# Kernel optimization log

Hardware: AMD Instinct MI355X
Metric: run time of the kernel (lower is better)

Reference implementation:

```python
import jax, jax.numpy as jnp
import numpy as np

B, G, N, C = 4, 64, 256, 256
HEAD = 8
HD = C // HEAD  # 32


def setup_inputs() -> dict:
    key = jax.random.key(0)
    ks = jax.random.split(key, 11)
    s = 0.02
    return {
        "q": jax.random.normal(ks[0], (B, G, N, C), jnp.float32),
        "k": jax.random.normal(ks[1], (B, G, N, C), jnp.float32),
        "v": jax.random.normal(ks[2], (B, G, N, C), jnp.float32),
        "wq": jax.random.normal(ks[3], (C, C), jnp.float32) * s,
        "bq": jnp.zeros((C,), jnp.float32),
        "wk": jax.random.normal(ks[4], (C, C), jnp.float32) * s,
        "bk": jnp.zeros((C,), jnp.float32),
        "wv": jax.random.normal(ks[5], (C, C), jnp.float32) * s,
        "bv": jnp.zeros((C,), jnp.float32),
        "wo": jax.random.normal(ks[6], (C, C), jnp.float32) * s,
        "bo": jnp.zeros((C,), jnp.float32),
    }


def reference(q, k, v, wq, bq, wk, bk, wv, bv, wo, bo):
    # Linear projections (torch Linear == x @ W.T + b; here W stored as (in,out))
    Q = q @ wq + bq  # (B,G,N,C)
    K = k @ wk + bk
    V = v @ wv + bv
    # split heads: (B,G,N,C) -> (B,G,N,H,hd)
    Qh = Q.reshape(B, G, N, HEAD, HD)
    Kh = K.reshape(B, G, N, HEAD, HD)
    Vh = V.reshape(B, G, N, HEAD, HD)
    scale = jnp.sqrt(jnp.float32(HD)) + 1e-8
    # scores: per batch b, head h, group g: (N,N)
    score = jnp.einsum("bgnhd,bgmhd->bhgnm", Qh, Kh) / scale
    attn = jax.nn.softmax(score, axis=-1)
    ctx = jnp.einsum("bhgnm,bgmhd->bgnhd", attn, Vh)  # (B,G,N,H,hd)
    ctx = ctx.reshape(B, G, N, C)
    # output projection (dropout = identity in eval)
    return ctx @ wo + bo
```

## Files before the change

### kernel.cpp

```cpp
#include <hip/hip_runtime.h>
#include <hip/hip_bf16.h>
#include <cstdint>
#include <cstddef>


typedef __attribute__((ext_vector_type(4))) float f4;
typedef __attribute__((ext_vector_type(8))) short s8;
typedef __attribute__((ext_vector_type(4))) short s4;
typedef unsigned short u16;

#define AS1 __attribute__((address_space(1)))
#define AS3 __attribute__((address_space(3)))

static constexpr int CD = 256;

__device__ __forceinline__ u16 f2bf(float f) {
    __hip_bfloat16 h = __float2bfloat16(f);
    return *reinterpret_cast<u16*>(&h);
}

__device__ __forceinline__ void gload_lds16(const void* g, void* l) {
    __builtin_amdgcn_global_load_lds((const AS1 uint32_t*)g, (AS3 uint32_t*)l, 16, 0, 0);
}

__global__ __launch_bounds__(256) void prep_k(const float* __restrict__ wq,
                                              const float* __restrict__ wk,
                                              const float* __restrict__ wv,
                                              const float* __restrict__ wo,
                                              u16* __restrict__ WT, float qs)
{
    const int bx = blockIdx.x;
    const int wsel = bx >> 4, tl = bx & 15;
    const int k0 = (tl & 3) * 64, n0 = (tl >> 2) * 64;
    const float* W = wsel == 0 ? wq : wsel == 1 ? wk : wsel == 2 ? wv : wo;
    const float scale = wsel == 0 ? qs : 1.0f;
    u16* dst = WT + (size_t)wsel * 65536;
    __shared__ float T[64][65];
    const int t = threadIdx.x;
    const int rr = t >> 4, c0 = (t & 15) * 4;
    #pragma unroll
    for (int i = 0; i < 4; ++i) {
        int r = i * 16 + rr;
        f4 f = *(const f4*)(W + (size_t)(k0 + r) * CD + n0 + c0);
        #pragma unroll
        for (int j = 0; j < 4; ++j) T[c0 + j][r] = f[j] * scale;
    }
    __syncthreads();
    #pragma unroll
    for (int i = 0; i < 4; ++i) {
        int n = i * 16 + rr;
        s4 h;
        #pragma unroll
        for (int j = 0; j < 4; ++j) h[j] = (short)f2bf(T[n][c0 + j]);
        *(s4*)(dst + (size_t)(n0 + n) * CD + k0 + c0) = h;
    }
}

template<bool A_F32, bool OUT_F32>
__device__ __forceinline__ void gemm_body(const void* __restrict__ Ain,
                                          const u16* __restrict__ Wt,
                                          const float* __restrict__ bias,
                                          float escale, void* __restrict__ Out,
                                          int d)
{
    __shared__ u16 As[128 * 64];
    __shared__ u16 Bs[128 * 64];
    const int n0 = (d >> 9) * 128;
    const int m0 = (d & 511) * 128;
    const int t = threadIdx.x, lane = t & 63, w = t >> 6;
    const int wr = (w >> 1) * 64, wc = (w & 1) * 64;
    const int lr = lane & 15, lk = (lane >> 4) * 8;

    f4 acc[4][4] = {};

    for (int k0 = 0; k0 < CD; k0 += 64) {
        #pragma unroll
        for (int j = 0; j < 4; ++j) {
            int c = j * 4 + w;
            int row = c * 8 + (lane >> 3);
            int col = ((lane & 7) * 8) ^ ((row & 7) << 3);
            gload_lds16(Wt + (size_t)(n0 + row) * CD + k0 + col,
                        &Bs[c * 512 + lane * 8]);
        }
        if constexpr (A_F32) {
            const float* A = (const float*)Ain;
            #pragma unroll
            for (int j = 0; j < 4; ++j) {
                int ch = t + j * 256;
                int r = ch >> 3, c8 = ch & 7;
                const float* src = A + (size_t)(m0 + r) * CD + k0 + c8 * 8;
                f4 f0 = *(const f4*)src;
                f4 f1 = *(const f4*)(src + 4);
                s8 h;
                #pragma unroll
                for (int i = 0; i < 4; ++i) {
                    h[i]     = (short)f2bf(f0[i]);
                    h[i + 4] = (short)f2bf(f1[i]);
                }
                *(s8*)&As[r * 64 + ((c8 * 8) ^ ((r & 7) << 3))] = h;
            }
        } else {
            const u16* A = (const u16*)Ain;
            #pragma unroll
            for (int j = 0; j < 4; ++j) {
                int c = j * 4 + w;
                int row = c * 8 + (lane >> 3);
                int col = ((lane & 7) * 8) ^ ((row & 7) << 3);
                gload_lds16(A + (size_t)(m0 + row) * CD + k0 + col,
                            &As[c * 512 + lane * 8]);
            }
        }
        __syncthreads();

        #pragma unroll
        for (int kk = 0; kk < 64; kk += 32) {
            s8 a[4], b[4];
            #pragma unroll
            for (int m = 0; m < 4; ++m) {
                int R = wr + m * 16 + lr;
                a[m] = *(const s8*)&As[R * 64 + ((kk + lk) ^ ((R & 7) << 3))];
            }
            #pragma unroll
            for (int n = 0; n < 4; ++n) {
                int R = wc + n * 16 + lr;
                b[n] = *(const s8*)&Bs[R * 64 + ((kk + lk) ^ ((R & 7) << 3))];
            }
            #pragma unroll
            for (int m = 0; m < 4; ++m)
                #pragma unroll
                for (int n = 0; n < 4; ++n)
                    acc[m][n] = __builtin_amdgcn_mfma_f32_16x16x32_bf16(
                        a[m], b[n], acc[m][n], 0, 0, 0);
        }
        __syncthreads();
    }

    const int orow = (lane >> 4) * 4;
    #pragma unroll
    for (int n = 0; n < 4; ++n) {
        int col = n0 + wc + n * 16 + lr;
        float bb = bias[col] * escale;
        #pragma unroll
        for (int m = 0; m < 4; ++m)
            #pragma unroll
            for (int r = 0; r < 4; ++r) {
                int row = m0 + wr + m * 16 + orow + r;
                float v = acc[m][n][r] + bb;
                if constexpr (OUT_F32)
                    ((float*)Out)[(size_t)row * CD + col] = v;
                else
                    ((u16*)Out)[(size_t)row * CD + col] = f2bf(v);
            }
    }
}

__global__ __launch_bounds__(256, 3) void gemmqkv_k(const float* q, const float* k,
        const float* v, const u16* WT, const float* bq, const float* bk,
        const float* bv, float qs, u16* Qb, u16* Kb, u16* Vb)
{
    const int op = blockIdx.x >> 10;
    const int d  = blockIdx.x & 1023;
    const float* A    = op == 0 ? q  : op == 1 ? k  : v;
    const u16*   Wt   = WT + (size_t)op * 65536;
    const float* bias = op == 0 ? bq : op == 1 ? bk : bv;
    u16*         Out  = op == 0 ? Qb : op == 1 ? Kb : Vb;
    gemm_body<true, false>(A, Wt, bias, op == 0 ? qs : 1.0f, Out, d);
}

__global__ __launch_bounds__(256, 3) void gemmo_k(const u16* Cx, const u16* WT,
                                                  const float* bo, float* out)
{
    gemm_body<false, true>(Cx, WT, bo, 1.0f, out, blockIdx.x);
}

__global__ __launch_bounds__(256, 3) void attn_k(const u16* Qb,
                                                 const u16* __restrict__ Kb,
                                                 const u16* __restrict__ Vb,
                                                 u16* Ctx)
{
    __shared__ u16 Ks[256 * 32];
    __shared__ u16 Vt[32][260];
    __shared__ u16 Ps[4][16][132];
    const int d = blockIdx.x;
    const int bg = d & 255, h = d >> 8;
    const size_t base = (size_t)bg * (256 * 256) + h * 32;
    const int t = threadIdx.x, lane = t & 63, w = t >> 6;
    const int lr = lane & 15, lk = (lane >> 4) * 8;
    const int orow = (lane >> 4) * 4;

    #pragma unroll
    for (int j = 0; j < 4; ++j) {
        int c = j * 4 + w;
        int row = c * 16 + (lane >> 2);
        int col = ((lane & 3) * 8) ^ (((row >> 1) & 3) << 3);
        gload_lds16(Kb + base + (size_t)row * CD + col, &Ks[c * 512 + lane * 8]);
    }
    {
        int n0 = (t >> 2) * 4, c0 = (t & 3) * 8;
        const u16* vp = Vb + base + (size_t)n0 * CD + c0;
        s8 r0 = *(const s8*)(vp);
        s8 r1 = *(const s8*)(vp + CD);
        s8 r2 = *(const s8*)(vp + 2 * CD);
        s8 r3 = *(const s8*)(vp + 3 * CD);
        #pragma unroll
        for (int i = 0; i < 8; ++i) {
            s4 cv = { r0[i], r1[i], r2[i], r3[i] };
            *(s4*)&Vt[c0 + i][n0] = cv;
        }
    }
    s8 aq[4];
    #pragma unroll
    for (int m = 0; m < 4; ++m)
        aq[m] = *(const s8*)(Qb + base + (size_t)(w * 64 + m * 16 + lr) * CD + lk);

    __syncthreads();

    const int myslot = lk ^ (((lr >> 1) & 3) << 3);
    const f4 zero = {0.f, 0.f, 0.f, 0.f};

    #pragma unroll
    for (int m = 0; m < 4; ++m) {
        f4 s[16];
        #pragma unroll
        for (int j = 0; j < 16; ++j) {
            s8 bk = *(const s8*)&Ks[(j * 16 + lr) * 32 + myslot];
            s[j] = __builtin_amdgcn_mfma_f32_16x16x32_bf16(aq[m], bk, zero, 0, 0, 0);
        }
        float mrow[4] = {-3.0e38f, -3.0e38f, -3.0e38f, -3.0e38f};
        #pragma unroll
        for (int j = 0; j < 16; ++j)
            #pragma unroll
            for (int r = 0; r < 4; ++r) mrow[r] = fmaxf(mrow[r], s[j][r]);
        #pragma unroll
        for (int dd = 1; dd < 16; dd <<= 1)
            #pragma unroll
            for (int r = 0; r < 4; ++r) mrow[r] = fmaxf(mrow[r], __shfl_xor(mrow[r], dd));
        float lsum[4] = {0.f, 0.f, 0.f, 0.f};
        #pragma unroll
        for (int j = 0; j < 16; ++j)
            #pragma unroll
            for (int r = 0; r < 4; ++r) {
                float p = exp2f(s[j][r] - mrow[r]);
                s[j][r] = p;
                lsum[r] += p;
            }
        #pragma unroll
        for (int dd = 1; dd < 16; dd <<= 1)
            #pragma unroll
            for (int r = 0; r < 4; ++r) lsum[r] += __shfl_xor(lsum[r], dd);

        f4 o0 = zero, o1 = zero;
        #pragma unroll
        for (int half = 0; half < 2; ++half) {
            #pragma unroll
            for (int j = 0; j < 8; ++j)
                #pragma unroll
                for (int r = 0; r < 4; ++r)
                    Ps[w][orow + r][j * 16 + lr] = f2bf(s[half * 8 + j][r]);
            #pragma unroll
            for (int kk = 0; kk < 4; ++kk) {
                s8 ap  = *(const s8*)&Ps[w][lr][kk * 32 + lk];
                s8 bv0 = *(const s8*)&Vt[lr][(half * 4 + kk) * 32 + lk];
                s8 bv1 = *(const s8*)&Vt[16 + lr][(half * 4 + kk) * 32 + lk];
                o0 = __builtin_amdgcn_mfma_f32_16x16x32_bf16(ap, bv0, o0, 0, 0, 0);
                o1 = __builtin_amdgcn_mfma_f32_16x16x32_bf16(ap, bv1, o1, 0, 0, 0);
            }
        }
        #pragma unroll
        for (int r = 0; r < 4; ++r) {
            float inv = __builtin_amdgcn_rcpf(lsum[r]);
            int row = w * 64 + m * 16 + orow + r;
            Ctx[base + (size_t)row * CD + lr]      = f2bf(o0[r] * inv);
            Ctx[base + (size_t)row * CD + 16 + lr] = f2bf(o1[r] * inv);
        }
    }
}

extern "C" void kernel_launch(void* const* d_in, const int* in_sizes, int n_in,
                              void* d_out, int out_size, void* d_ws, size_t ws_size,
                              hipStream_t stream) {
    const float* q  = (const float*)d_in[0];
    const float* k  = (const float*)d_in[1];
    const float* v  = (const float*)d_in[2];
    const float* wq = (const float*)d_in[3];
    const float* bq = (const float*)d_in[4];
    const float* wk = (const float*)d_in[5];
    const float* bk = (const float*)d_in[6];
    const float* wv = (const float*)d_in[7];
    const float* bv = (const float*)d_in[8];
    const float* wo = (const float*)d_in[9];
    const float* bo = (const float*)d_in[10];
    float* out = (float*)d_out;

    const size_t E = (size_t)65536 * 256;
    u16* Qb = (u16*)d_ws;
    u16* Kb = Qb + E;
    u16* Vb = Kb + E;
    u16* WT = Vb + E;
    u16* Cx = Qb;

    const float qs = (1.0f / (sqrtf(32.0f) + 1e-8f)) * 1.4426950408889634f;

    prep_k<<<64, 256, 0, stream>>>(wq, wk, wv, wo, WT, qs);
    gemmqkv_k<<<3072, 256, 0, stream>>>(q, k, v, WT, bq, bk, bv, qs, Qb, Kb, Vb);
    attn_k<<<2048, 256, 0, stream>>>(Qb, Kb, Vb, Cx);
    gemmo_k<<<1024, 256, 0, stream>>>(Cx, WT + 3 * 65536, bo, out);
}
```

Measured before the change: 186.1 us.

## Restructure projection GEMMs to full-K weight tile in LDS with direct A loads

The projection GEMM now loads the whole 64-column weight slab for the full K=256 into LDS once, in an MFMA-friendly layout. A operands stream straight from global memory into registers with two-step register prefetching, replacing the per-K-step LDS staging and barriers. Tiles shrink to 128x64, which doubles grid sizes, and block ordering is interleaved so neighbouring blocks share A rows for L2 reuse. Launch bounds go up to 4 waves per SIMD. In exchange, weights are re-read by more blocks and the A register loads are less coalesced.

New measurement: 241.9 us. 30.0% more time.

```diff
diff --git a/kernel.cpp b/kernel.cpp
--- a/kernel.cpp
+++ b/kernel.cpp
@@ -63,103 +63,112 @@
                                           float escale, void* __restrict__ Out,
                                           int d)
 {
-    __shared__ u16 As[128 * 64];
-    __shared__ u16 Bs[128 * 64];
-    const int n0 = (d >> 9) * 128;
-    const int m0 = (d & 511) * 128;
+    __shared__ u16 Bs[32 * 64 * 8];
     const int t = threadIdx.x, lane = t & 63, w = t >> 6;
-    const int wr = (w >> 1) * 64, wc = (w & 1) * 64;
-    const int lr = lane & 15, lk = (lane >> 4) * 8;
-
-    f4 acc[4][4] = {};
-
-    for (int k0 = 0; k0 < CD; k0 += 64) {
-        #pragma unroll
-        for (int j = 0; j < 4; ++j) {
-            int c = j * 4 + w;
-            int row = c * 8 + (lane >> 3);
-            int col = ((lane & 7) * 8) ^ ((row & 7) << 3);
-            gload_lds16(Wt + (size_t)(n0 + row) * CD + k0 + col,
-                        &Bs[c * 512 + lane * 8]);
-        }
-        if constexpr (A_F32) {
-            const float* A = (const float*)Ain;
-            #pragma unroll
-            for (int j = 0; j < 4; ++j) {
-                int ch = t + j * 256;
-                int r = ch >> 3, c8 = ch & 7;
-                const float* src = A + (size_t)(m0 + r) * CD + k0 + c8 * 8;
-                f4 f0 = *(const f4*)src;
-                f4 f1 = *(const f4*)(src + 4);
-                s8 h;
-                #pragma unroll
-                for (int i = 0; i < 4; ++i) {
-                    h[i]     = (short)f2bf(f0[i]);
-                    h[i + 4] = (short)f2bf(f1[i]);
-                }
-                *(s8*)&As[r * 64 + ((c8 * 8) ^ ((r & 7) << 3))] = h;
-            }
-        } else {
-            const u16* A = (const u16*)Ain;
-            #pragma unroll
-            for (int j = 0; j < 4; ++j) {
-                int c = j * 4 + w;
-                int row = c * 8 + (lane >> 3);
-                int col = ((lane & 7) * 8) ^ ((row & 7) << 3);
-                gload_lds16(A + (size_t)(m0 + row) * CD + k0 + col,
-                            &As[c * 512 + lane * 8]);
-            }
-        }
-        __syncthreads();
-
-        #pragma unroll
-        for (int kk = 0; kk < 64; kk += 32) {
-            s8 a[4], b[4];
-            #pragma unroll
-            for (int m = 0; m < 4; ++m) {
-                int R = wr + m * 16 + lr;
-                a[m] = *(const s8*)&As[R * 64 + ((kk + lk) ^ ((R & 7) << 3))];
+    const int n0 = ((d >> 3) & 3) * 64;
+    const int m0 = (((d >> 5) << 3) | (d & 7)) * 128;
+    const int lr = lane & 15, lkg = lane >> 4;
+
+    {
+        int col = t >> 2, g = t & 3;
+        const u16* src = Wt + (size_t)(n0 + col) * CD + g * 64;
+        #pragma unroll
+        for (int j = 0; j < 8; ++j) {
+            int s = g * 8 + j;
+            *(s8*)&Bs[(s * 64 + col) * 8] = *(const s8*)(src + j * 8);
+        }
+    }
+    __syncthreads();
+
+    const int rowA = m0 + w * 32 + lr;
+    f4 acc[2][4] = {};
+
+    if constexpr (A_F32) {
+        const float* A = (const float*)Ain;
+        const float* ap0 = A + (size_t)rowA * CD + lkg * 8;
+        const float* ap1 = ap0 + (size_t)16 * CD;
+        f4 pf[2][4];
+        #pragma unroll
+        for (int i = 0; i < 2; ++i) {
+            pf[i][0] = *(const f4*)(ap0 + i * 32);
+            pf[i][1] = *(const f4*)(ap0 + i * 32 + 4);
+            pf[i][2] = *(const f4*)(ap1 + i * 32);
+            pf[i][3] = *(const f4*)(ap1 + i * 32 + 4);
+        }
+        #pragma unroll
+        for (int ks = 0; ks < 8; ++ks) {
+            s8 a0, a1;
+            #pragma unroll
+            for (int i = 0; i < 4; ++i) {
+                a0[i]     = (short)f2bf(pf[ks & 1][0][i]);
+                a0[i + 4] = (short)f2bf(pf[ks & 1][1][i]);
+                a1[i]     = (short)f2bf(pf[ks & 1][2][i]);
+                a1[i + 4] = (short)f2bf(pf[ks & 1][3][i]);
+            }
+            if (ks < 6) {
+                pf[ks & 1][0] = *(const f4*)(ap0 + (ks + 2) * 32);
+                pf[ks & 1][1] = *(const f4*)(ap0 + (ks + 2) * 32 + 4);
+                pf[ks & 1][2] = *(const f4*)(ap1 + (ks + 2) * 32);
+                pf[ks & 1][3] = *(const f4*)(ap1 + (ks + 2) * 32 + 4);
             }
             #pragma unroll
             for (int n = 0; n < 4; ++n) {
-                int R = wc + n * 16 + lr;
-                b[n] = *(const s8*)&Bs[R * 64 + ((kk + lk) ^ ((R & 7) << 3))];
-            }
-            #pragma unroll
-            for (int m = 0; m < 4; ++m)
-                #pragma unroll
-                for (int n = 0; n < 4; ++n)
-                    acc[m][n] = __builtin_amdgcn_mfma_f32_16x16x32_bf16(
-                        a[m], b[n], acc[m][n], 0, 0, 0);
-        }
-        __syncthreads();
-    }
-
-    const int orow = (lane >> 4) * 4;
+                s8 b = *(const s8*)&Bs[((ks * 4 + lkg) * 64 + n * 16 + lr) * 8];
+                acc[0][n] = __builtin_amdgcn_mfma_f32_16x16x32_bf16(a0, b, acc[0][n], 0, 0, 0);
+                acc[1][n] = __builtin_amdgcn_mfma_f32_16x16x32_bf16(a1, b, acc[1][n], 0, 0, 0);
+            }
+        }
+    } else {
+        const u16* A = (const u16*)Ain;
+        const u16* ap0 = A + (size_t)rowA * CD + lkg * 8;
+        const u16* ap1 = ap0 + (size_t)16 * CD;
+        s8 pf[2][2];
+        #pragma unroll
+        for (int i = 0; i < 2; ++i) {
+            pf[i][0] = *(const s8*)(ap0 + i * 32);
+            pf[i][1] = *(const s8*)(ap1 + i * 32);
+        }
+        #pragma unroll
+        for (int ks = 0; ks < 8; ++ks) {
+            s8 a0 = pf[ks & 1][0], a1 = pf[ks & 1][1];
+            if (ks < 6) {
+                pf[ks & 1][0] = *(const s8*)(ap0 + (ks + 2) * 32);
+                pf[ks & 1][1] = *(const s8*)(ap1 + (ks + 2) * 32);
+            }
+            #pragma unroll
+            for (int n = 0; n < 4; ++n) {
+                s8 b = *(const s8*)&Bs[((ks * 4 + lkg) * 64 + n * 16 + lr) * 8];
+                acc[0][n] = __builtin_amdgcn_mfma_f32_16x16x32_bf16(a0, b, acc[0][n], 0, 0, 0);
+                acc[1][n] = __builtin_amdgcn_mfma_f32_16x16x32_bf16(a1, b, acc[1][n], 0, 0, 0);
+            }
+        }
+    }
+
+    const int orow = lkg * 4;
     #pragma unroll
     for (int n = 0; n < 4; ++n) {
-        int col = n0 + wc + n * 16 + lr;
+        int col = n0 + n * 16 + lr;
         float bb = bias[col] * escale;
         #pragma unroll
-        for (int m = 0; m < 4; ++m)
+        for (int m = 0; m < 2; ++m)
             #pragma unroll
             for (int r = 0; r < 4; ++r) {
-                int row = m0 + wr + m * 16 + orow + r;
-                float v = acc[m][n][r] + bb;
+                int row = m0 + w * 32 + m * 16 + orow + r;
+                float vv = acc[m][n][r] + bb;
                 if constexpr (OUT_F32)
-                    ((float*)Out)[(size_t)row * CD + col] = v;
+                    ((float*)Out)[(size_t)row * CD + col] = vv;
                 else
-                    ((u16*)Out)[(size_t)row * CD + col] = f2bf(v);
-            }
-    }
-}
-
-__global__ __launch_bounds__(256, 3) void gemmqkv_k(const float* q, const float* k,
+                    ((u16*)Out)[(size_t)row * CD + col] = f2bf(vv);
+            }
+    }
+}
+
+__global__ __launch_bounds__(256, 4) void gemmqkv_k(const float* q, const float* k,
         const float* v, const u16* WT, const float* bq, const float* bk,
         const float* bv, float qs, u16* Qb, u16* Kb, u16* Vb)
 {
-    const int op = blockIdx.x >> 10;
-    const int d  = blockIdx.x & 1023;
+    const int op = blockIdx.x >> 11;
+    const int d  = blockIdx.x & 2047;
     const float* A    = op == 0 ? q  : op == 1 ? k  : v;
     const u16*   Wt   = WT + (size_t)op * 65536;
     const float* bias = op == 0 ? bq : op == 1 ? bk : bv;
@@ -167,7 +176,7 @@
     gemm_body<true, false>(A, Wt, bias, op == 0 ? qs : 1.0f, Out, d);
 }
 
-__global__ __launch_bounds__(256, 3) void gemmo_k(const u16* Cx, const u16* WT,
+__global__ __launch_bounds__(256, 4) void gemmo_k(const u16* Cx, const u16* WT,
                                                   const float* bo, float* out)
 {
     gemm_body<false, true>(Cx, WT, bo, 1.0f, out, blockIdx.x);
@@ -302,7 +311,7 @@
     const float qs = (1.0f / (sqrtf(32.0f) + 1e-8f)) * 1.4426950408889634f;
 
     prep_k<<<64, 256, 0, stream>>>(wq, wk, wv, wo, WT, qs);
-    gemmqkv_k<<<3072, 256, 0, stream>>>(q, k, v, WT, bq, bk, bv, qs, Qb, Kb, Vb);
+    gemmqkv_k<<<6144, 256, 0, stream>>>(q, k, v, WT, bq, bk, bv, qs, Qb, Kb, Vb);
     attn_k<<<2048, 256, 0, stream>>>(Qb, Kb, Vb, Cx);
-    gemmo_k<<<1024, 256, 0, stream>>>(Cx, WT + 3 * 65536, bo, out);
-}
+    gemmo_k<<<2048, 256, 0, stream>>>(Cx, WT + 3 * 65536, bo, out);
+}
```

## Double-buffer GEMM k-tiles with register prefetch of fp32 A operand

Applied to the files above, without the earlier changes.

Both GEMM kernels now keep two LDS buffers for the A and B tiles and issue the loads for the next 64-wide k-tile before the MFMA loop on the current tile. The fp32 input is held in registers during compute and converted and written to LDS afterwards. This aims to hide global load latency behind matrix math and removes one barrier per iteration. It doubles LDS use to 64KB per block and adds registers for the prefetch, so launch bounds drop from 3 to 2 blocks per CU, which reduces occupancy.

Measured after the change: 193.8 us. 1.04x slower.

```diff
diff --git a/kernel.cpp b/kernel.cpp
--- a/kernel.cpp
+++ b/kernel.cpp
@@ -63,67 +63,77 @@
                                           float escale, void* __restrict__ Out,
                                           int d)
 {
-    __shared__ u16 As[128 * 64];
-    __shared__ u16 Bs[128 * 64];
+    __shared__ u16 As[2][128 * 64];
+    __shared__ u16 Bs[2][128 * 64];
+    const int t = threadIdx.x, lane = t & 63, w = t >> 6;
     const int n0 = (d >> 9) * 128;
     const int m0 = (d & 511) * 128;
-    const int t = threadIdx.x, lane = t & 63, w = t >> 6;
     const int wr = (w >> 1) * 64, wc = (w & 1) * 64;
     const int lr = lane & 15, lk = (lane >> 4) * 8;
+    const int bc = lane >> 3, bcol = (lane & 7) * 8;
 
     f4 acc[4][4] = {};
-
-    for (int k0 = 0; k0 < CD; k0 += 64) {
+    f4 pa[8];
+
+    auto stageB = [&](int k0, int buf) {
         #pragma unroll
         for (int j = 0; j < 4; ++j) {
             int c = j * 4 + w;
-            int row = c * 8 + (lane >> 3);
-            int col = ((lane & 7) * 8) ^ ((row & 7) << 3);
+            int row = c * 8 + bc;
+            int col = bcol ^ ((row & 7) << 3);
             gload_lds16(Wt + (size_t)(n0 + row) * CD + k0 + col,
-                        &Bs[c * 512 + lane * 8]);
-        }
-        if constexpr (A_F32) {
-            const float* A = (const float*)Ain;
-            #pragma unroll
-            for (int j = 0; j < 4; ++j) {
-                int ch = t + j * 256;
-                int r = ch >> 3, c8 = ch & 7;
-                const float* src = A + (size_t)(m0 + r) * CD + k0 + c8 * 8;
-                f4 f0 = *(const f4*)src;
-                f4 f1 = *(const f4*)(src + 4);
-                s8 h;
-                #pragma unroll
-                for (int i = 0; i < 4; ++i) {
-                    h[i]     = (short)f2bf(f0[i]);
-                    h[i + 4] = (short)f2bf(f1[i]);
-                }
-                *(s8*)&As[r * 64 + ((c8 * 8) ^ ((r & 7) << 3))] = h;
-            }
-        } else {
-            const u16* A = (const u16*)Ain;
-            #pragma unroll
-            for (int j = 0; j < 4; ++j) {
-                int c = j * 4 + w;
-                int row = c * 8 + (lane >> 3);
-                int col = ((lane & 7) * 8) ^ ((row & 7) << 3);
-                gload_lds16(A + (size_t)(m0 + row) * CD + k0 + col,
-                            &As[c * 512 + lane * 8]);
-            }
-        }
-        __syncthreads();
-
+                        &Bs[buf][c * 512 + lane * 8]);
+        }
+    };
+    auto stageA16 = [&](int k0, int buf) {
+        const u16* A = (const u16*)Ain;
+        #pragma unroll
+        for (int j = 0; j < 4; ++j) {
+            int c = j * 4 + w;
+            int row = c * 8 + bc;
+            int col = bcol ^ ((row & 7) << 3);
+            gload_lds16(A + (size_t)(m0 + row) * CD + k0 + col,
+                        &As[buf][c * 512 + lane * 8]);
+        }
+    };
+    auto loadA = [&](int k0) {
+        const float* A = (const float*)Ain;
+        #pragma unroll
+        for (int j = 0; j < 4; ++j) {
+            int ch = t + j * 256;
+            int r = ch >> 3, c8 = ch & 7;
+            const float* src = A + (size_t)(m0 + r) * CD + k0 + c8 * 8;
+            pa[2 * j]     = *(const f4*)src;
+            pa[2 * j + 1] = *(const f4*)(src + 4);
+        }
+    };
+    auto writeA = [&](int buf) {
+        #pragma unroll
+        for (int j = 0; j < 4; ++j) {
+            int ch = t + j * 256;
+            int r = ch >> 3, c8 = ch & 7;
+            s8 h;
+            #pragma unroll
+            for (int i = 0; i < 4; ++i) {
+                h[i]     = (short)f2bf(pa[2 * j][i]);
+                h[i + 4] = (short)f2bf(pa[2 * j + 1][i]);
+            }
+            *(s8*)&As[buf][r * 64 + ((c8 * 8) ^ ((r & 7) << 3))] = h;
+        }
+    };
+    auto compute = [&](int buf) {
         #pragma unroll
         for (int kk = 0; kk < 64; kk += 32) {
             s8 a[4], b[4];
             #pragma unroll
             for (int m = 0; m < 4; ++m) {
                 int R = wr + m * 16 + lr;
-                a[m] = *(const s8*)&As[R * 64 + ((kk + lk) ^ ((R & 7) << 3))];
+                a[m] = *(const s8*)&As[buf][R * 64 + ((kk + lk) ^ ((R & 7) << 3))];
             }
             #pragma unroll
             for (int n = 0; n < 4; ++n) {
                 int R = wc + n * 16 + lr;
-                b[n] = *(const s8*)&Bs[R * 64 + ((kk + lk) ^ ((R & 7) << 3))];
+                b[n] = *(const s8*)&Bs[buf][R * 64 + ((kk + lk) ^ ((R & 7) << 3))];
             }
             #pragma unroll
             for (int m = 0; m < 4; ++m)
@@ -132,6 +142,24 @@
                     acc[m][n] = __builtin_amdgcn_mfma_f32_16x16x32_bf16(
                         a[m], b[n], acc[m][n], 0, 0, 0);
         }
+    };
+
+    stageB(0, 0);
+    if constexpr (A_F32) { loadA(0); writeA(0); } else { stageA16(0, 0); }
+    __syncthreads();
+
+    #pragma unroll
+    for (int ti = 0; ti < 4; ++ti) {
+        const int cur = ti & 1, nxt = cur ^ 1;
+        const int kn = (ti + 1) * 64;
+        if (ti < 3) {
+            if constexpr (A_F32) loadA(kn); else stageA16(kn, nxt);
+            stageB(kn, nxt);
+        }
+        compute(cur);
+        if (ti < 3) {
+            if constexpr (A_F32) writeA(nxt);
+        }
         __syncthreads();
     }
 
@@ -145,16 +173,16 @@
             #pragma unroll
             for (int r = 0; r < 4; ++r) {
                 int row = m0 + wr + m * 16 + orow + r;
-                float v = acc[m][n][r] + bb;
+                float vv = acc[m][n][r] + bb;
                 if constexpr (OUT_F32)
-                    ((float*)Out)[(size_t)row * CD + col] = v;
+                    ((float*)Out)[(size_t)row * CD + col] = vv;
                 else
-                    ((u16*)Out)[(size_t)row * CD + col] = f2bf(v);
-            }
-    }
-}
-
-__global__ __launch_bounds__(256, 3) void gemmqkv_k(const float* q, const float* k,
+                    ((u16*)Out)[(size_t)row * CD + col] = f2bf(vv);
+            }
+    }
+}
+
+__global__ __launch_bounds__(256, 2) void gemmqkv_k(const float* q, const float* k,
         const float* v, const u16* WT, const float* bq, const float* bk,
         const float* bv, float qs, u16* Qb, u16* Kb, u16* Vb)
 {
@@ -167,7 +195,7 @@
     gemm_body<true, false>(A, Wt, bias, op == 0 ? qs : 1.0f, Out, d);
 }
 
-__global__ __launch_bounds__(256, 3) void gemmo_k(const u16* Cx, const u16* WT,
+__global__ __launch_bounds__(256, 2) void gemmo_k(const u16* Cx, const u16* WT,
                                                   const float* bo, float* out)
 {
     gemm_body<false, true>(Cx, WT, bo, 1.0f, out, blockIdx.x);
```
